# Optimization experiments

Measured on AMD Instinct MI355X. Metric: run time of the kernel, lower is better.

The kernel has to match this reference:

```python
import jax, jax.numpy as jnp
import numpy as np

VOCAB = 200000
EMB = 128
HID = 128
NT = 16
B = 4096


def setup_inputs() -> dict:
    key = jax.random.key(0)
    ks = jax.random.split(key, 8)
    x = jax.random.randint(ks[0], (B, 1), 0, VOCAB, dtype=jnp.int64)
    emb = jax.random.normal(ks[1], (VOCAB, EMB), dtype=jnp.float32) * 0.02
    emb = emb.at[0].set(0.0)  # padding_idx=0
    s = 1.0 / np.sqrt(HID)
    w_ih = jax.random.uniform(ks[2], (4 * HID, EMB), minval=-s, maxval=s, dtype=jnp.float32)
    w_hh = jax.random.uniform(ks[3], (4 * HID, HID), minval=-s, maxval=s, dtype=jnp.float32)
    b_ih = jax.random.uniform(ks[4], (4 * HID,), minval=-s, maxval=s, dtype=jnp.float32)
    b_hh = jax.random.uniform(ks[5], (4 * HID,), minval=-s, maxval=s, dtype=jnp.float32)
    w_fc = jax.random.uniform(ks[6], (NT, HID), minval=-s, maxval=s, dtype=jnp.float32)
    b_fc = jax.random.uniform(ks[7], (NT,), minval=-s, maxval=s, dtype=jnp.float32)
    return {"x": x, "emb": emb, "w_ih": w_ih, "w_hh": w_hh,
            "b_ih": b_ih, "b_hh": b_hh, "w_fc": w_fc, "b_fc": b_fc}


def _lstm(xs, w_ih, w_hh, b_ih, b_hh):
    # xs: [T, E]; torch LSTM with batch=1, gate order i, f, g, o
    H = HID
    b = b_ih + b_hh

    def step(carry, xt):
        h, c = carry
        z = xt @ w_ih.T + h @ w_hh.T + b  # [4H]
        i = jax.nn.sigmoid(z[:H])
        f = jax.nn.sigmoid(z[H:2 * H])
        g = jnp.tanh(z[2 * H:3 * H])
        o = jax.nn.sigmoid(z[3 * H:])
        c = f * c + i * g
        h = o * jnp.tanh(c)
        return (h, c), h

    init = (jnp.zeros((H,), xs.dtype), jnp.zeros((H,), xs.dtype))
    _, hs = jax.lax.scan(step, init, xs)
    return hs  # [T, H]


def reference(x, emb, w_ih, w_hh, b_ih, b_hh, w_fc, b_fc):
    emb = emb.at[0].set(0.0)  # padding_idx=0
    xe = emb[x[:, 0]]  # [B, E] == lstm input viewed as (seq=B, batch=1, E)
    hs = _lstm(xe, w_ih, w_hh, b_ih, b_hh)  # [B, H]
    out = hs @ w_fc.T + b_fc  # [B, NT]; torch .squeeze(1) is a no-op for NT>1
    return out
```

## Files before the change

### kernel.cpp

```cpp
#include <hip/hip_runtime.h>
#include <math.h>

#define EMBD 128
#define HIDD 128
#define NTAR 16
#define BSEQ 4096
#define G4   512
#define CH   8

typedef _Float16 v2h __attribute__((ext_vector_type(2)));

#define DPP_ADD(x, ctrl)                                                     \
    ((x) + __int_as_float(__builtin_amdgcn_update_dpp(                       \
               0, __float_as_int(x), (ctrl), 0xf, 0xf, true)))
#define DPP_BCAST(x, ctrl)                                                   \
    (__int_as_float(__builtin_amdgcn_update_dpp(                             \
         0, __float_as_int(x), (ctrl), 0xf, 0xf, true)))

__device__ __forceinline__ float fast_tanh(float z) {
    return 1.f - 2.f * __builtin_amdgcn_rcpf(1.f + __expf(2.f * z));
}

__device__ __forceinline__ v2h pack_f16(float f0, float f1) {
    return __builtin_bit_cast(v2h, __builtin_amdgcn_cvt_pkrtz(f0, f1));
}

__global__ void input_proj_kernel(const int* __restrict__ x,
                                  const float* __restrict__ emb,
                                  const float* __restrict__ w_ih,
                                  const float* __restrict__ b_ih,
                                  const float* __restrict__ b_hh,
                                  float* __restrict__ zxT) {
    const int t = blockIdx.x;
    const int j = threadIdx.x;
    const int u = j >> 2;
    const int g = j & 3;
    const int row = g * HIDD + u;
    const int idx = x[t];
    const float4* __restrict__ er = (const float4*)(emb + (long long)idx * EMBD);
    const float4* __restrict__ wr = (const float4*)(w_ih + row * EMBD);
    float acc = 0.f;
#pragma unroll
    for (int k = 0; k < EMBD / 4; ++k) {
        float4 e = er[k];
        float4 w = wr[k];
        acc += e.x * w.x + e.y * w.y + e.z * w.z + e.w * w.w;
    }
    zxT[(t * HIDD + u) * 4 + g] = acc + b_ih[row] + b_hh[row];
}

__global__ __launch_bounds__(512, 2)
void lstm_seq_kernel(const float* __restrict__ zxT,
                     const float* __restrict__ w_hh,
                     float* __restrict__ hs) {
    __shared__ __align__(16) _Float16 h_db[2][HIDD];

    const int tid = threadIdx.x;
    const int l   = tid & 63;
    const int wv  = tid >> 6;
    const int kq  = l & 3;
    const int us  = l >> 2;
    const int u   = wv * 16 + us;
    const bool writer = (kq == 0);

    const float mA = (kq == 2) ? 2.f : -1.f;
    const float cA = (kq == 2) ? -2.f : 1.f;
    const float cB = (kq == 2) ? 1.f : 0.f;

    v2h w2h[4][16];
#pragma unroll
    for (int g = 0; g < 4; ++g) {
        const float* __restrict__ wr = w_hh + (g * HIDD + u) * HIDD + 32 * kq;
#pragma unroll
        for (int j = 0; j < 4; ++j) {
            const int c0 = 8 * ((j + kq) & 3);
#pragma unroll
            for (int p = 0; p < 4; ++p) {
                const float f0 = wr[c0 + 2 * p];
                const float f1 = wr[c0 + 2 * p + 1];
                w2h[g][4 * j + p] = pack_f16(f0, f1);
            }
        }
    }
#pragma unroll
    for (int g = 0; g < 4; ++g)
#pragma unroll
        for (int k = 0; k < 16; ++k)
            asm volatile("" : "+v"(w2h[g][k]));

    if (tid < HIDD) {
        h_db[0][tid] = (_Float16)0.f;
        h_db[1][tid] = (_Float16)0.f;
    }
    float c = 0.f;
    float hreg[CH];
    float zcur[CH], zfut[CH];
    const int zoff = wv * 64 + l;
#pragma unroll
    for (int s = 0; s < CH; ++s) {
        zcur[s] = zxT[s * G4 + zoff];
        hreg[s] = 0.f;
    }
    __syncthreads();

    for (int tc = 0; tc < BSEQ; tc += CH) {
        if (writer && tc > 0) {
#pragma unroll
            for (int s = 0; s < CH; ++s)
                hs[(tc - CH + s) * HIDD + u] = hreg[s];
        }
        {
            const int tn = (tc + CH < BSEQ) ? (tc + CH) : (BSEQ - CH);
#pragma unroll
            for (int s = 0; s < CH; ++s)
                zfut[s] = zxT[(tn + s) * G4 + zoff];
        }

#pragma unroll
        for (int s = 0; s < CH; ++s) {
            const uint4* __restrict__ rb =
                (const uint4*)(&h_db[s & 1][32 * kq]);
            const int wb = (s & 1) ^ 1;

            float z0a = 0.f, z1a = 0.f, z2a = 0.f, z3a = 0.f;
            float z0b = 0.f, z1b = 0.f, z2b = 0.f, z3b = 0.f;
#pragma unroll
            for (int j = 0; j < 4; ++j) {
                const int cj = (j + kq) & 3;
                const uint4 hb = rb[cj];
                v2h hp[4];
                hp[0] = __builtin_bit_cast(v2h, hb.x);
                hp[1] = __builtin_bit_cast(v2h, hb.y);
                hp[2] = __builtin_bit_cast(v2h, hb.z);
                hp[3] = __builtin_bit_cast(v2h, hb.w);
                if (j < 2) {
#pragma unroll
                    for (int p = 0; p < 4; ++p) {
                        z0a = __builtin_amdgcn_fdot2(hp[p], w2h[0][4 * j + p], z0a, false);
                        z1a = __builtin_amdgcn_fdot2(hp[p], w2h[1][4 * j + p], z1a, false);
                        z2a = __builtin_amdgcn_fdot2(hp[p], w2h[2][4 * j + p], z2a, false);
                        z3a = __builtin_amdgcn_fdot2(hp[p], w2h[3][4 * j + p], z3a, false);
                    }
                } else {
#pragma unroll
                    for (int p = 0; p < 4; ++p) {
                        z0b = __builtin_amdgcn_fdot2(hp[p], w2h[0][4 * j + p], z0b, false);
                        z1b = __builtin_amdgcn_fdot2(hp[p], w2h[1][4 * j + p], z1b, false);
                        z2b = __builtin_amdgcn_fdot2(hp[p], w2h[2][4 * j + p], z2b, false);
                        z3b = __builtin_amdgcn_fdot2(hp[p], w2h[3][4 * j + p], z3b, false);
                    }
                }
            }
            float z0 = z0a + z0b, z1 = z1a + z1b;
            float z2 = z2a + z2b, z3 = z3a + z3b;

            z0 = DPP_ADD(z0, 0xB1); z0 = DPP_ADD(z0, 0x4E);
            z1 = DPP_ADD(z1, 0xB1); z1 = DPP_ADD(z1, 0x4E);
            z2 = DPP_ADD(z2, 0xB1); z2 = DPP_ADD(z2, 0x4E);
            z3 = DPP_ADD(z3, 0xB1); z3 = DPP_ADD(z3, 0x4E);

            float zs = z0;
            zs = (kq == 1) ? z1 : zs;
            zs = (kq == 2) ? z2 : zs;
            zs = (kq == 3) ? z3 : zs;
            const float zfull = zs + zcur[s];
            const float r   = __builtin_amdgcn_rcpf(1.f + __expf(mA * zfull));
            const float act = fmaf(cA, r, cB);

            const float gi = DPP_BCAST(act, 0x00);
            const float gf = DPP_BCAST(act, 0x55);
            const float gg = DPP_BCAST(act, 0xAA);
            const float go = DPP_BCAST(act, 0xFF);

            c = gf * c + gi * gg;
            const float h = go * fast_tanh(c);
            hreg[s] = h;
            if (writer) h_db[wb][u] = (_Float16)h;
            __syncthreads();
        }
#pragma unroll
        for (int s = 0; s < CH; ++s) zcur[s] = zfut[s];
    }
    if (writer) {
#pragma unroll
        for (int s = 0; s < CH; ++s)
            hs[(BSEQ - CH + s) * HIDD + u] = hreg[s];
    }
}

__global__ void fc_kernel(const float* __restrict__ hs,
                          const float* __restrict__ w_fc,
                          const float* __restrict__ b_fc,
                          float* __restrict__ out) {
    const int gid = blockIdx.x * blockDim.x + threadIdx.x;
    if (gid >= BSEQ * NTAR) return;
    const int n = gid & (NTAR - 1);
    const int t = gid >> 4;
    const float4* __restrict__ hr = (const float4*)(hs + t * HIDD);
    const float4* __restrict__ wr = (const float4*)(w_fc + n * HIDD);
    float acc = 0.f;
#pragma unroll
    for (int k = 0; k < HIDD / 4; ++k) {
        float4 h = hr[k];
        float4 wv = wr[k];
        acc += h.x * wv.x + h.y * wv.y + h.z * wv.z + h.w * wv.w;
    }
    out[gid] = acc + b_fc[n];
}

extern "C" void kernel_launch(void* const* d_in, const int* in_sizes, int n_in,
                              void* d_out, int out_size, void* d_ws, size_t ws_size,
                              hipStream_t stream) {
    const int*   x    = (const int*)d_in[0];
    const float* emb  = (const float*)d_in[1];
    const float* w_ih = (const float*)d_in[2];
    const float* w_hh = (const float*)d_in[3];
    const float* b_ih = (const float*)d_in[4];
    const float* b_hh = (const float*)d_in[5];
    const float* w_fc = (const float*)d_in[6];
    const float* b_fc = (const float*)d_in[7];
    float* out = (float*)d_out;

    float* zxT = (float*)d_ws;
    float* hs  = zxT + (size_t)BSEQ * G4;

    input_proj_kernel<<<BSEQ, G4, 0, stream>>>(x, emb, w_ih, b_ih, b_hh, zxT);
    lstm_seq_kernel<<<1, 512, 0, stream>>>(zxT, w_hh, hs);
    fc_kernel<<<(BSEQ * NTAR + 255) / 256, 256, 0, stream>>>(hs, w_fc, b_fc, out);
}
```

Measured before the change: 2.367 ms.

## Halve LSTM recurrence block to 256 threads with two hidden units per thread

The sequential LSTM kernel now runs with 4 waves instead of 8, and each thread computes two hidden units. Each thread therefore holds twice as many fp16 weight registers and twice as many dot products per step. The aim is to make the per-timestep __syncthreads barrier cheaper and to increase instruction-level parallelism within a wave. In exchange, each step's critical path carries roughly double the arithmetic per wave, and register pressure goes up (128 packed weight registers).

```diff
diff --git a/kernel.cpp b/kernel.cpp
--- a/kernel.cpp
+++ b/kernel.cpp
@@ -20,7 +20,6 @@
 __device__ __forceinline__ float fast_tanh(float z) {
     return 1.f - 2.f * __builtin_amdgcn_rcpf(1.f + __expf(2.f * z));
 }
-
 __device__ __forceinline__ v2h pack_f16(float f0, float f1) {
     return __builtin_bit_cast(v2h, __builtin_amdgcn_cvt_pkrtz(f0, f1));
 }
@@ -49,7 +48,7 @@
     zxT[(t * HIDD + u) * 4 + g] = acc + b_ih[row] + b_hh[row];
 }
 
-__global__ __launch_bounds__(512, 2)
+__global__ __launch_bounds__(256, 1)
 void lstm_seq_kernel(const float* __restrict__ zxT,
                      const float* __restrict__ w_hh,
                      float* __restrict__ hs) {
@@ -60,60 +59,73 @@
     const int wv  = tid >> 6;
     const int kq  = l & 3;
     const int us  = l >> 2;
-    const int u   = wv * 16 + us;
+    const int u0  = wv * 32 + us;
+    const int u1  = u0 + 16;
     const bool writer = (kq == 0);
 
     const float mA = (kq == 2) ? 2.f : -1.f;
     const float cA = (kq == 2) ? -2.f : 1.f;
     const float cB = (kq == 2) ? 1.f : 0.f;
 
-    v2h w2h[4][16];
-#pragma unroll
-    for (int g = 0; g < 4; ++g) {
-        const float* __restrict__ wr = w_hh + (g * HIDD + u) * HIDD + 32 * kq;
-#pragma unroll
-        for (int j = 0; j < 4; ++j) {
-            const int c0 = 8 * ((j + kq) & 3);
-#pragma unroll
-            for (int p = 0; p < 4; ++p) {
-                const float f0 = wr[c0 + 2 * p];
-                const float f1 = wr[c0 + 2 * p + 1];
-                w2h[g][4 * j + p] = pack_f16(f0, f1);
-            }
-        }
-    }
-#pragma unroll
-    for (int g = 0; g < 4; ++g)
-#pragma unroll
-        for (int k = 0; k < 16; ++k)
-            asm volatile("" : "+v"(w2h[g][k]));
+    v2h w2h[2][4][16];
+#pragma unroll
+    for (int un = 0; un < 2; ++un) {
+        const int u = un ? u1 : u0;
+#pragma unroll
+        for (int g = 0; g < 4; ++g) {
+            const float* __restrict__ wr =
+                w_hh + (g * HIDD + u) * HIDD + 32 * kq;
+#pragma unroll
+            for (int j = 0; j < 4; ++j) {
+                const int c0 = 8 * ((j + kq) & 3);
+#pragma unroll
+                for (int p = 0; p < 4; ++p)
+                    w2h[un][g][4 * j + p] =
+                        pack_f16(wr[c0 + 2 * p], wr[c0 + 2 * p + 1]);
+            }
+        }
+    }
+#pragma unroll
+    for (int un = 0; un < 2; ++un)
+#pragma unroll
+        for (int g = 0; g < 4; ++g)
+#pragma unroll
+            for (int k = 0; k < 16; ++k)
+                asm volatile("" : "+v"(w2h[un][g][k]));
 
     if (tid < HIDD) {
         h_db[0][tid] = (_Float16)0.f;
         h_db[1][tid] = (_Float16)0.f;
     }
-    float c = 0.f;
-    float hreg[CH];
-    float zcur[CH], zfut[CH];
-    const int zoff = wv * 64 + l;
+    float c0r = 0.f, c1r = 0.f;
+    float hreg0[CH], hreg1[CH];
+    float zcur0[CH], zcur1[CH], zfut0[CH], zfut1[CH];
+    const int zoff0 = wv * 128 + l;
+    const int zoff1 = zoff0 + 64;
 #pragma unroll
     for (int s = 0; s < CH; ++s) {
-        zcur[s] = zxT[s * G4 + zoff];
-        hreg[s] = 0.f;
+        zcur0[s] = zxT[s * G4 + zoff0];
+        zcur1[s] = zxT[s * G4 + zoff1];
+        hreg0[s] = 0.f;
+        hreg1[s] = 0.f;
     }
     __syncthreads();
 
     for (int tc = 0; tc < BSEQ; tc += CH) {
         if (writer && tc > 0) {
 #pragma unroll
-            for (int s = 0; s < CH; ++s)
-                hs[(tc - CH + s) * HIDD + u] = hreg[s];
+            for (int s = 0; s < CH; ++s) {
+                hs[(tc - CH + s) * HIDD + u0] = hreg0[s];
+                hs[(tc - CH + s) * HIDD + u1] = hreg1[s];
+            }
         }
         {
             const int tn = (tc + CH < BSEQ) ? (tc + CH) : (BSEQ - CH);
 #pragma unroll
-            for (int s = 0; s < CH; ++s)
-                zfut[s] = zxT[(tn + s) * G4 + zoff];
+            for (int s = 0; s < CH; ++s) {
+                zfut0[s] = zxT[(tn + s) * G4 + zoff0];
+                zfut1[s] = zxT[(tn + s) * G4 + zoff1];
+            }
         }
 
 #pragma unroll
@@ -122,8 +134,8 @@
                 (const uint4*)(&h_db[s & 1][32 * kq]);
             const int wb = (s & 1) ^ 1;
 
-            float z0a = 0.f, z1a = 0.f, z2a = 0.f, z3a = 0.f;
-            float z0b = 0.f, z1b = 0.f, z2b = 0.f, z3b = 0.f;
+            float za[2][4] = {{0.f,0.f,0.f,0.f},{0.f,0.f,0.f,0.f}};
+            float zbb[2][4] = {{0.f,0.f,0.f,0.f},{0.f,0.f,0.f,0.f}};
 #pragma unroll
             for (int j = 0; j < 4; ++j) {
                 const int cj = (j + kq) & 3;
@@ -135,56 +147,81 @@
                 hp[3] = __builtin_bit_cast(v2h, hb.w);
                 if (j < 2) {
 #pragma unroll
-                    for (int p = 0; p < 4; ++p) {
-                        z0a = __builtin_amdgcn_fdot2(hp[p], w2h[0][4 * j + p], z0a, false);
-                        z1a = __builtin_amdgcn_fdot2(hp[p], w2h[1][4 * j + p], z1a, false);
-                        z2a = __builtin_amdgcn_fdot2(hp[p], w2h[2][4 * j + p], z2a, false);
-                        z3a = __builtin_amdgcn_fdot2(hp[p], w2h[3][4 * j + p], z3a, false);
-                    }
+                    for (int p = 0; p < 4; ++p)
+#pragma unroll
+                        for (int un = 0; un < 2; ++un)
+#pragma unroll
+                            for (int g = 0; g < 4; ++g)
+                                za[un][g] = __builtin_amdgcn_fdot2(
+                                    hp[p], w2h[un][g][4 * j + p], za[un][g], false);
                 } else {
 #pragma unroll
-                    for (int p = 0; p < 4; ++p) {
-                        z0b = __builtin_amdgcn_fdot2(hp[p], w2h[0][4 * j + p], z0b, false);
-                        z1b = __builtin_amdgcn_fdot2(hp[p], w2h[1][4 * j + p], z1b, false);
-                        z2b = __builtin_amdgcn_fdot2(hp[p], w2h[2][4 * j + p], z2b, false);
-                        z3b = __builtin_amdgcn_fdot2(hp[p], w2h[3][4 * j + p], z3b, false);
-                    }
+                    for (int p = 0; p < 4; ++p)
+#pragma unroll
+                        for (int un = 0; un < 2; ++un)
+#pragma unroll
+                            for (int g = 0; g < 4; ++g)
+                                zbb[un][g] = __builtin_amdgcn_fdot2(
+                                    hp[p], w2h[un][g][4 * j + p], zbb[un][g], false);
                 }
             }
-            float z0 = z0a + z0b, z1 = z1a + z1b;
-            float z2 = z2a + z2b, z3 = z3a + z3b;
-
-            z0 = DPP_ADD(z0, 0xB1); z0 = DPP_ADD(z0, 0x4E);
-            z1 = DPP_ADD(z1, 0xB1); z1 = DPP_ADD(z1, 0x4E);
-            z2 = DPP_ADD(z2, 0xB1); z2 = DPP_ADD(z2, 0x4E);
-            z3 = DPP_ADD(z3, 0xB1); z3 = DPP_ADD(z3, 0x4E);
-
-            float zs = z0;
-            zs = (kq == 1) ? z1 : zs;
-            zs = (kq == 2) ? z2 : zs;
-            zs = (kq == 3) ? z3 : zs;
-            const float zfull = zs + zcur[s];
-            const float r   = __builtin_amdgcn_rcpf(1.f + __expf(mA * zfull));
-            const float act = fmaf(cA, r, cB);
-
-            const float gi = DPP_BCAST(act, 0x00);
-            const float gf = DPP_BCAST(act, 0x55);
-            const float gg = DPP_BCAST(act, 0xAA);
-            const float go = DPP_BCAST(act, 0xFF);
-
-            c = gf * c + gi * gg;
-            const float h = go * fast_tanh(c);
-            hreg[s] = h;
-            if (writer) h_db[wb][u] = (_Float16)h;
+            float z0[4], z1[4];
+#pragma unroll
+            for (int g = 0; g < 4; ++g) {
+                z0[g] = za[0][g] + zbb[0][g];
+                z1[g] = za[1][g] + zbb[1][g];
+            }
+
+#pragma unroll
+            for (int g = 0; g < 4; ++g) {
+                z0[g] = DPP_ADD(z0[g], 0xB1); z0[g] = DPP_ADD(z0[g], 0x4E);
+                z1[g] = DPP_ADD(z1[g], 0xB1); z1[g] = DPP_ADD(z1[g], 0x4E);
+            }
+
+            float zs0 = z0[0], zs1 = z1[0];
+            zs0 = (kq == 1) ? z0[1] : zs0;  zs1 = (kq == 1) ? z1[1] : zs1;
+            zs0 = (kq == 2) ? z0[2] : zs0;  zs1 = (kq == 2) ? z1[2] : zs1;
+            zs0 = (kq == 3) ? z0[3] : zs0;  zs1 = (kq == 3) ? z1[3] : zs1;
+            const float zf0 = zs0 + zcur0[s];
+            const float zf1 = zs1 + zcur1[s];
+            const float r0   = __builtin_amdgcn_rcpf(1.f + __expf(mA * zf0));
+            const float r1   = __builtin_amdgcn_rcpf(1.f + __expf(mA * zf1));
+            const float act0 = fmaf(cA, r0, cB);
+            const float act1 = fmaf(cA, r1, cB);
+
+            const float gi0 = DPP_BCAST(act0, 0x00);
+            const float gf0 = DPP_BCAST(act0, 0x55);
+            const float gg0 = DPP_BCAST(act0, 0xAA);
+            const float go0 = DPP_BCAST(act0, 0xFF);
+            const float gi1 = DPP_BCAST(act1, 0x00);
+            const float gf1 = DPP_BCAST(act1, 0x55);
+            const float gg1 = DPP_BCAST(act1, 0xAA);
+            const float go1 = DPP_BCAST(act1, 0xFF);
+
+            c0r = gf0 * c0r + gi0 * gg0;
+            c1r = gf1 * c1r + gi1 * gg1;
+            const float h0 = go0 * fast_tanh(c0r);
+            const float h1 = go1 * fast_tanh(c1r);
+            hreg0[s] = h0;
+            hreg1[s] = h1;
+            if (writer) {
+                h_db[wb][u0] = (_Float16)h0;
+                h_db[wb][u1] = (_Float16)h1;
+            }
             __syncthreads();
         }
 #pragma unroll
-        for (int s = 0; s < CH; ++s) zcur[s] = zfut[s];
+        for (int s = 0; s < CH; ++s) {
+            zcur0[s] = zfut0[s];
+            zcur1[s] = zfut1[s];
+        }
     }
     if (writer) {
 #pragma unroll
-        for (int s = 0; s < CH; ++s)
-            hs[(BSEQ - CH + s) * HIDD + u] = hreg[s];
+        for (int s = 0; s < CH; ++s) {
+            hs[(BSEQ - CH + s) * HIDD + u0] = hreg0[s];
+            hs[(BSEQ - CH + s) * HIDD + u1] = hreg1[s];
+        }
     }
 }
 
@@ -225,6 +262,6 @@
     float* hs  = zxT + (size_t)BSEQ * G4;
 
     input_proj_kernel<<<BSEQ, G4, 0, stream>>>(x, emb, w_ih, b_ih, b_hh, zxT);
-    lstm_seq_kernel<<<1, 512, 0, stream>>>(zxT, w_hh, hs);
+    lstm_seq_kernel<<<1, 256, 0, stream>>>(zxT, w_hh, hs);
     fc_kernel<<<(BSEQ * NTAR + 255) / 256, 256, 0, stream>>>(hs, w_fc, b_fc, out);
 }
```

After: 2.489 ms. 1.05x slower.
